# Optimization experiments

Hardware: AMD Instinct MI355X
Metric: run time of the kernel (lower is better)

The kernel has to match this reference:

```python
import jax, jax.numpy as jnp
import numpy as np

# dims
B, T = 64, 512
L = 3                 # number of HMLSTM layers
IN = 512              # per-layer input size (all equal)
D = L * IN            # 1536 total input size
E = 1024              # embedding_size
H1, H2 = 1024, 1024   # linear_sizes
O = 512               # output_size


def setup_inputs() -> dict:
    key = jax.random.key(0)
    ks = jax.random.split(key, 12)
    s = 0.02
    return {
        "x": jax.random.normal(ks[0], (B, T, D), dtype=jnp.float32),
        # gate linears: Linear(sum(input_sizes) -> 1, bias=False), one per layer, stacked [L, D]
        "Wg": jax.random.normal(ks[1], (L, D), dtype=jnp.float32) * s,
        # per-layer embedding linears Linear(IN -> E), stacked [L, E, IN] / [L, E]
        "We": jax.random.normal(ks[2], (L, E, IN), dtype=jnp.float32) * s,
        "be": jax.random.normal(ks[3], (L, E), dtype=jnp.float32) * s,
        # tanh MLP stack
        "W1": jax.random.normal(ks[4], (H1, E), dtype=jnp.float32) * s,
        "b1": jax.random.normal(ks[5], (H1,), dtype=jnp.float32) * s,
        "W2": jax.random.normal(ks[6], (H2, H1), dtype=jnp.float32) * s,
        "b2": jax.random.normal(ks[7], (H2,), dtype=jnp.float32) * s,
        # output head
        "Wo": jax.random.normal(ks[8], (O, H2), dtype=jnp.float32) * s,
        "bo": jax.random.normal(ks[9], (O,), dtype=jnp.float32) * s,
    }


def reference(x, Wg, We, be, W1, b1, W2, b2, Wo, bo):
    b, t, d = x.shape
    h = x.reshape(b * t, d)                       # per-timestep features, fully batched over time
    # gates: sigmoid(Linear(full h -> 1)) per layer -> [N, L]
    g = jax.nn.sigmoid(h @ Wg.T)
    # split full input into per-layer chunks (equal sizes -> reshape) and gate them
    hl = h.reshape(b * t, L, IN) * g[:, :, None]  # [N, L, IN]
    # s = sum_l Linear_l(h_l * g_l); biases sum since each embedding adds its own bias
    s = jnp.einsum("nli,lei->ne", hl, We) + be.sum(axis=0)
    he = jax.nn.relu(s)
    # fnn: tanh-activated linear stack
    o = jnp.tanh(he @ W1.T + b1)
    o = jnp.tanh(o @ W2.T + b2)
    out = o @ Wo.T + bo
    return out.reshape(b, t, O)
```

## Files before the change

### kernel.cpp

```cpp
#include <hip/hip_runtime.h>
#include <math.h>


typedef __attribute__((ext_vector_type(8))) short short8;
typedef __attribute__((ext_vector_type(4))) float float4v;

#define DEV __device__ __forceinline__

DEV unsigned short f2bf(float f){
    union{float f; unsigned int i;} c; c.f = f;
    unsigned int r = c.i + 0x7fffu + ((c.i>>16)&1u);
    return (unsigned short)(r>>16);
}
DEV unsigned int pack2(float a, float b){
    return (unsigned int)f2bf(a) | ((unsigned int)f2bf(b)<<16);
}

DEV void gload_lds16(const unsigned short* g, unsigned short* l){
    __builtin_amdgcn_global_load_lds((const __attribute__((address_space(1))) void*)g,
                                     (__attribute__((address_space(3))) void*)l, 16, 0, 0);
}

__global__ __launch_bounds__(256) void cvt_flat(const float* __restrict__ src,
                                                unsigned short* __restrict__ dst, int n8)
{
    int v = blockIdx.x*256 + threadIdx.x;
    if(v >= n8) return;
    const float4* s = (const float4*)(src) + v*2;
    float4 a = s[0], b = s[1];
    uint4 o;
    o.x = pack2(a.x, a.y); o.y = pack2(a.z, a.w);
    o.z = pack2(b.x, b.y); o.w = pack2(b.z, b.w);
    *((uint4*)dst + v) = o;
}

__global__ __launch_bounds__(256) void cvt_we(const float* __restrict__ We,
                                              unsigned short* __restrict__ Wep)
{
    int v  = blockIdx.x*256 + threadIdx.x;
    int i8 = v & 63;
    int e  = (v>>6) & 1023;
    int l  = v>>16;
    const float4* s = (const float4*)(We + (size_t)l*524288 + (size_t)e*512 + i8*8);
    float4 a = s[0], b = s[1];
    uint4 o;
    o.x = pack2(a.x, a.y); o.y = pack2(a.z, a.w);
    o.z = pack2(b.x, b.y); o.w = pack2(b.z, b.w);
    *(uint4*)(Wep + (size_t)e*1536 + (size_t)l*512 + i8*8) = o;
}

__global__ __launch_bounds__(256) void gate_u(const float* __restrict__ x,
                                              const float* __restrict__ Wg,
                                              unsigned short* __restrict__ u)
{
    int row  = blockIdx.x*4 + (threadIdx.x>>6);
    int lane = threadIdx.x & 63;
    const float4* xr = (const float4*)(x + (size_t)row*1536);
    float4 hv[6];
    #pragma unroll
    for(int j=0;j<6;j++) hv[j] = xr[j*64 + lane];

    float p[3];
    #pragma unroll
    for(int l=0;l<3;l++){
        const float4* wr = (const float4*)(Wg + (size_t)l*1536);
        float s = 0.f;
        #pragma unroll
        for(int j=0;j<6;j++){
            float4 wv = wr[j*64 + lane];
            s += hv[j].x*wv.x + hv[j].y*wv.y + hv[j].z*wv.z + hv[j].w*wv.w;
        }
        p[l] = s;
    }
    #pragma unroll
    for(int off=32; off; off>>=1){
        p[0] += __shfl_xor(p[0], off);
        p[1] += __shfl_xor(p[1], off);
        p[2] += __shfl_xor(p[2], off);
    }
    float g[3];
    #pragma unroll
    for(int l=0;l<3;l++) g[l] = 1.f/(1.f + __expf(-p[l]));

    uint2* ur = (uint2*)(u + (size_t)row*1536);
    #pragma unroll
    for(int j=0;j<6;j++){
        float gj = g[(j*64+lane)>>7];
        uint2 o;
        o.x = pack2(hv[j].x*gj, hv[j].y*gj);
        o.y = pack2(hv[j].z*gj, hv[j].w*gj);
        ur[j*64 + lane] = o;
    }
}

template<int ACT, int BIAS_ROWS, bool F32OUT>
__global__ __launch_bounds__(256) void gemm_bt(
    const unsigned short* __restrict__ A,
    const unsigned short* __restrict__ W,
    const float* __restrict__ bias,
    void* __restrict__ Cv,
    int M, int N, int K)
{
    __shared__ __align__(128) unsigned short As[128*64];
    __shared__ __align__(128) unsigned short Bs[128*64];

    int tid = threadIdx.x;
    int nb  = N >> 7;
    int mt  = M >> 7;
    int xcd = blockIdx.x & 7;
    int j   = blockIdx.x >> 3;
    int bm  = xcd*(mt>>3) + j/nb;
    int bn  = j % nb;
    int m0  = bm << 7, n0 = bn << 7;

    int lane = tid & 63, wv = tid >> 6;
    int wm = wv >> 1, wn = wv & 1;
    int lr = lane & 15, quad = lane >> 4;

    float4v acc[4][4];
    #pragma unroll
    for(int i=0;i<4;i++)
        #pragma unroll
        for(int jj=0;jj<4;jj++) acc[i][jj] = (float4v){0.f,0.f,0.f,0.f};

    int rl  = lane >> 3;
    int cbs = (lane & 7) ^ rl;
    const unsigned short* gA = A + ((size_t)m0 + wv*32 + rl)*K + cbs*8;
    const unsigned short* gB = W + ((size_t)n0 + wv*32 + rl)*K + cbs*8;
    const size_t rstep = (size_t)8*K;

    for(int k0=0; k0<K; k0+=64){
        #pragma unroll
        for(int d=0; d<4; d++){
            gload_lds16(gA + d*rstep, &As[(wv*32 + d*8)*64]);
            gload_lds16(gB + d*rstep, &Bs[(wv*32 + d*8)*64]);
        }
        gA += 64; gB += 64;
        __syncthreads();

        #pragma unroll
        for(int ks=0; ks<2; ks++){
            short8 af[4], bfr[4];
            #pragma unroll
            for(int mi=0;mi<4;mi++){
                int row = wm*64 + mi*16 + lr;
                int cbx = (ks*4 + quad) ^ (lr & 7);
                af[mi] = *(const short8*)(&As[row*64 + cbx*8]);
            }
            #pragma unroll
            for(int ni=0;ni<4;ni++){
                int row = wn*64 + ni*16 + lr;
                int cbx = (ks*4 + quad) ^ (lr & 7);
                bfr[ni] = *(const short8*)(&Bs[row*64 + cbx*8]);
            }
            #pragma unroll
            for(int mi=0;mi<4;mi++)
                #pragma unroll
                for(int ni=0;ni<4;ni++)
                    acc[mi][ni] = __builtin_amdgcn_mfma_f32_16x16x32_bf16(af[mi], bfr[ni], acc[mi][ni], 0, 0, 0);
        }
        __syncthreads();
    }

    #pragma unroll
    for(int ni=0;ni<4;ni++){
        int n = n0 + wn*64 + ni*16 + lr;
        float bsum = 0.f;
        #pragma unroll
        for(int r=0;r<BIAS_ROWS;r++) bsum += bias[(size_t)r*N + n];
        #pragma unroll
        for(int mi=0;mi<4;mi++){
            #pragma unroll
            for(int reg=0;reg<4;reg++){
                int m = m0 + wm*64 + mi*16 + quad*4 + reg;
                float v = acc[mi][ni][reg] + bsum;
                if(ACT==1)      v = fmaxf(v, 0.f);
                else if(ACT==2) v = tanhf(v);
                if constexpr (F32OUT) ((float*)Cv)[(size_t)m*N + n] = v;
                else                  ((unsigned short*)Cv)[(size_t)m*N + n] = f2bf(v);
            }
        }
    }
}

extern "C" void kernel_launch(void* const* d_in, const int* in_sizes, int n_in,
                              void* d_out, int out_size, void* d_ws, size_t ws_size,
                              hipStream_t stream)
{
    const float* x  = (const float*)d_in[0];
    const float* Wg = (const float*)d_in[1];
    const float* We = (const float*)d_in[2];
    const float* be = (const float*)d_in[3];
    const float* W1 = (const float*)d_in[4];
    const float* b1 = (const float*)d_in[5];
    const float* W2 = (const float*)d_in[6];
    const float* b2 = (const float*)d_in[7];
    const float* Wo = (const float*)d_in[8];
    const float* bo = (const float*)d_in[9];
    float* out = (float*)d_out;

    const int M = 32768;

    char* w = (char*)d_ws;
    unsigned short* Wep   = (unsigned short*)w; w += (size_t)1024*1536*2;
    unsigned short* W1b   = (unsigned short*)w; w += (size_t)1024*1024*2;
    unsigned short* W2b   = (unsigned short*)w; w += (size_t)1024*1024*2;
    unsigned short* Wob   = (unsigned short*)w; w += (size_t)512*1024*2;
    unsigned short* slotA = (unsigned short*)w; w += (size_t)M*1536*2;
    unsigned short* slotB = (unsigned short*)w; w += (size_t)M*1024*2;
    unsigned short* u  = slotA;
    unsigned short* o1 = slotA;
    unsigned short* he = slotB;
    unsigned short* o2 = slotB;

    hipLaunchKernelGGL(cvt_flat, dim3(512), dim3(256), 0, stream, W1, W1b, 131072);
    hipLaunchKernelGGL(cvt_flat, dim3(512), dim3(256), 0, stream, W2, W2b, 131072);
    hipLaunchKernelGGL(cvt_flat, dim3(256), dim3(256), 0, stream, Wo, Wob, 65536);
    hipLaunchKernelGGL(cvt_we,   dim3(768), dim3(256), 0, stream, We, Wep);

    hipLaunchKernelGGL(gate_u, dim3(M/4), dim3(256), 0, stream, x, Wg, u);
    hipLaunchKernelGGL((gemm_bt<1,3,false>), dim3((M/128)*(1024/128)), dim3(256), 0, stream,
                       u,  Wep, be, he,  M, 1024, 1536);
    hipLaunchKernelGGL((gemm_bt<2,1,false>), dim3((M/128)*(1024/128)), dim3(256), 0, stream,
                       he, W1b, b1, o1,  M, 1024, 1024);
    hipLaunchKernelGGL((gemm_bt<2,1,false>), dim3((M/128)*(1024/128)), dim3(256), 0, stream,
                       o1, W2b, b2, o2,  M, 1024, 1024);
    hipLaunchKernelGGL((gemm_bt<0,1,true>),  dim3((M/128)*(512/128)),  dim3(256), 0, stream,
                       o2, Wob, bo, out, M, 512, 1024);
}
```

Measured before the change: 729.0 us.

## Replace GEMM with 256x256 tiled, double-buffered, 8-wave pipelined kernel

Replaces the 128x128 single-buffered GEMM with a 256x256 tile kernel using 512 threads and two LDS stages. Global-to-LDS loads for the next one or two K steps are issued in chunks between MFMA groups, with fine-grained barriers, vmcnt waits and setprio. The aim is to hide memory latency behind MFMA work and raise data reuse per tile. The cost is more LDS per block (128 KB) and more register pressure, which may lower occupancy. The manual barrier and waitcnt ordering also needs care to stay correct.

```diff
diff --git a/kernel.cpp b/kernel.cpp
--- a/kernel.cpp
+++ b/kernel.cpp
@@ -94,86 +94,111 @@
 }
 
 template<int ACT, int BIAS_ROWS, bool F32OUT>
-__global__ __launch_bounds__(256) void gemm_bt(
+__global__ __launch_bounds__(512, 2) void gemm256(
     const unsigned short* __restrict__ A,
     const unsigned short* __restrict__ W,
     const float* __restrict__ bias,
     void* __restrict__ Cv,
     int M, int N, int K)
 {
-    __shared__ __align__(128) unsigned short As[128*64];
-    __shared__ __align__(128) unsigned short Bs[128*64];
-
-    int tid = threadIdx.x;
-    int nb  = N >> 7;
-    int mt  = M >> 7;
-    int xcd = blockIdx.x & 7;
-    int j   = blockIdx.x >> 3;
-    int bm  = xcd*(mt>>3) + j/nb;
-    int bn  = j % nb;
-    int m0  = bm << 7, n0 = bn << 7;
-
-    int lane = tid & 63, wv = tid >> 6;
-    int wm = wv >> 1, wn = wv & 1;
-    int lr = lane & 15, quad = lane >> 4;
-
-    float4v acc[4][4];
-    #pragma unroll
-    for(int i=0;i<4;i++)
+    __shared__ __align__(128) unsigned short As[2*2*128*64];
+    __shared__ __align__(128) unsigned short Bs[2*2*128*64];
+
+    const int tid = threadIdx.x;
+    const int nb  = N >> 8;
+    const int mt  = M >> 8;
+    const int xcd = blockIdx.x & 7;
+    const int j   = blockIdx.x >> 3;
+    const int bm  = xcd*(mt>>3) + j/nb;
+    const int bn  = j % nb;
+    const int m0  = bm << 8, n0 = bn << 8;
+
+    const int lane = tid & 63, wid = tid >> 6;
+    const int wm = wid >> 2, wn = wid & 3;
+    const int lr = lane & 15, quad = lane >> 4, sx = lr & 7;
+    const int srow = lane >> 3;
+    const int scb  = (lane & 7) ^ srow;
+    const size_t aoff = (size_t)srow*K + scb*8;
+    const int nt = K >> 6;
+
+    float4v acc[8][4];
+    #pragma unroll
+    for(int i=0;i<8;i++)
         #pragma unroll
         for(int jj=0;jj<4;jj++) acc[i][jj] = (float4v){0.f,0.f,0.f,0.f};
 
-    int rl  = lane >> 3;
-    int cbs = (lane & 7) ^ rl;
-    const unsigned short* gA = A + ((size_t)m0 + wv*32 + rl)*K + cbs*8;
-    const unsigned short* gB = W + ((size_t)n0 + wv*32 + rl)*K + cbs*8;
-    const size_t rstep = (size_t)8*K;
-
-    for(int k0=0; k0<K; k0+=64){
-        #pragma unroll
-        for(int d=0; d<4; d++){
-            gload_lds16(gA + d*rstep, &As[(wv*32 + d*8)*64]);
-            gload_lds16(gB + d*rstep, &Bs[(wv*32 + d*8)*64]);
+#define STAGE_A(h,l,s) gload_lds16(A + ((size_t)(m0 + (h)*128 + (l)*64 + wid*8))*K + (s)*64 + aoff, \
+                                   &As[(((s)&1)*2+(h))*8192 + ((l)*64 + wid*8)*64])
+#define STAGE_B(h,l,s) gload_lds16(W + ((size_t)(n0 + (h)*128 + (l)*64 + wid*8))*K + (s)*64 + aoff, \
+                                   &Bs[(((s)&1)*2+(h))*8192 + ((l)*64 + wid*8)*64])
+
+    STAGE_A(0,0,0); STAGE_A(0,1,0); STAGE_A(1,0,0); STAGE_A(1,1,0);
+    STAGE_B(0,0,0); STAGE_B(0,1,0); STAGE_B(1,0,0); STAGE_B(1,1,0);
+    if(nt > 1){
+        STAGE_B(0,0,1); STAGE_B(0,1,1); STAGE_B(1,0,1); STAGE_B(1,1,1);
+        STAGE_A(0,0,1); STAGE_A(1,0,1);
+        asm volatile("s_waitcnt vmcnt(6)" ::: "memory");
+    } else {
+        asm volatile("s_waitcnt vmcnt(0)" ::: "memory");
+    }
+    __builtin_amdgcn_s_barrier();
+
+    for(int t=0; t<nt; ++t){
+        const int cur = t & 1;
+        const unsigned short* Ab = &As[(cur*2 + wm)*8192];
+        const unsigned short* Bb = &Bs[(cur*2 + (wn>>1))*8192 + (wn&1)*4096];
+        short8 bfr[4][2];
+        #pragma unroll
+        for(int q=0; q<4; ++q){
+            short8 af[2][2];
+            #pragma unroll
+            for(int mi=0; mi<2; ++mi)
+                #pragma unroll
+                for(int ks=0; ks<2; ++ks)
+                    af[mi][ks] = *(const short8*)&Ab[(q*32 + mi*16 + lr)*64 + (((ks*4+quad)^sx)*8)];
+            if(q==0){
+                #pragma unroll
+                for(int ni=0; ni<4; ++ni)
+                    #pragma unroll
+                    for(int ks=0; ks<2; ++ks)
+                        bfr[ni][ks] = *(const short8*)&Bb[(ni*16 + lr)*64 + (((ks*4+quad)^sx)*8)];
+            }
+            if(q==0)      { if(t+1 < nt){ STAGE_A(0,1,t+1); STAGE_A(1,1,t+1); } }
+            else if(q==1) { if(t+2 < nt){ STAGE_B(0,0,t+2); STAGE_B(0,1,t+2); } }
+            else if(q==2) { if(t+2 < nt){ STAGE_B(1,0,t+2); STAGE_B(1,1,t+2); } }
+            else          { if(t+2 < nt){ STAGE_A(0,0,t+2); STAGE_A(1,0,t+2); } }
+            __builtin_amdgcn_s_barrier();
+            __builtin_amdgcn_s_setprio(1);
+            #pragma unroll
+            for(int ks=0; ks<2; ++ks)
+                #pragma unroll
+                for(int mi=0; mi<2; ++mi)
+                    #pragma unroll
+                    for(int ni=0; ni<4; ++ni)
+                        acc[q*2+mi][ni] = __builtin_amdgcn_mfma_f32_16x16x32_bf16(
+                            af[mi][ks], bfr[ni][ks], acc[q*2+mi][ni], 0, 0, 0);
+            __builtin_amdgcn_s_setprio(0);
+            if(q < 3) __builtin_amdgcn_s_barrier();
         }
-        gA += 64; gB += 64;
-        __syncthreads();
-
-        #pragma unroll
-        for(int ks=0; ks<2; ks++){
-            short8 af[4], bfr[4];
+        if(t+2 < nt) asm volatile("s_waitcnt vmcnt(6)" ::: "memory");
+        else         asm volatile("s_waitcnt vmcnt(0)" ::: "memory");
+        __builtin_amdgcn_s_barrier();
+    }
+#undef STAGE_A
+#undef STAGE_B
+
+    #pragma unroll
+    for(int ni=0; ni<4; ++ni){
+        const int n = n0 + wn*64 + ni*16 + lr;
+        float bsum = 0.f;
+        #pragma unroll
+        for(int r=0; r<BIAS_ROWS; ++r) bsum += bias[(size_t)r*N + n];
+        #pragma unroll
+        for(int Q=0; Q<8; ++Q){
             #pragma unroll
-            for(int mi=0;mi<4;mi++){
-                int row = wm*64 + mi*16 + lr;
-                int cbx = (ks*4 + quad) ^ (lr & 7);
-                af[mi] = *(const short8*)(&As[row*64 + cbx*8]);
-            }
-            #pragma unroll
-            for(int ni=0;ni<4;ni++){
-                int row = wn*64 + ni*16 + lr;
-                int cbx = (ks*4 + quad) ^ (lr & 7);
-                bfr[ni] = *(const short8*)(&Bs[row*64 + cbx*8]);
-            }
-            #pragma unroll
-            for(int mi=0;mi<4;mi++)
-                #pragma unroll
-                for(int ni=0;ni<4;ni++)
-                    acc[mi][ni] = __builtin_amdgcn_mfma_f32_16x16x32_bf16(af[mi], bfr[ni], acc[mi][ni], 0, 0, 0);
-        }
-        __syncthreads();
-    }
-
-    #pragma unroll
-    for(int ni=0;ni<4;ni++){
-        int n = n0 + wn*64 + ni*16 + lr;
-        float bsum = 0.f;
-        #pragma unroll
-        for(int r=0;r<BIAS_ROWS;r++) bsum += bias[(size_t)r*N + n];
-        #pragma unroll
-        for(int mi=0;mi<4;mi++){
-            #pragma unroll
-            for(int reg=0;reg<4;reg++){
-                int m = m0 + wm*64 + mi*16 + quad*4 + reg;
-                float v = acc[mi][ni][reg] + bsum;
+            for(int reg=0; reg<4; ++reg){
+                const int m = m0 + wm*128 + Q*16 + quad*4 + reg;
+                float v = acc[Q][ni][reg] + bsum;
                 if(ACT==1)      v = fmaxf(v, 0.f);
                 else if(ACT==2) v = tanhf(v);
                 if constexpr (F32OUT) ((float*)Cv)[(size_t)m*N + n] = v;
@@ -219,12 +244,12 @@
     hipLaunchKernelGGL(cvt_we,   dim3(768), dim3(256), 0, stream, We, Wep);
 
     hipLaunchKernelGGL(gate_u, dim3(M/4), dim3(256), 0, stream, x, Wg, u);
-    hipLaunchKernelGGL((gemm_bt<1,3,false>), dim3((M/128)*(1024/128)), dim3(256), 0, stream,
+    hipLaunchKernelGGL((gemm256<1,3,false>), dim3((M/256)*(1024/256)), dim3(512), 0, stream,
                        u,  Wep, be, he,  M, 1024, 1536);
-    hipLaunchKernelGGL((gemm_bt<2,1,false>), dim3((M/128)*(1024/128)), dim3(256), 0, stream,
+    hipLaunchKernelGGL((gemm256<2,1,false>), dim3((M/256)*(1024/256)), dim3(512), 0, stream,
                        he, W1b, b1, o1,  M, 1024, 1024);
-    hipLaunchKernelGGL((gemm_bt<2,1,false>), dim3((M/128)*(1024/128)), dim3(256), 0, stream,
+    hipLaunchKernelGGL((gemm256<2,1,false>), dim3((M/256)*(1024/256)), dim3(512), 0, stream,
                        o1, W2b, b2, o2,  M, 1024, 1024);
-    hipLaunchKernelGGL((gemm_bt<0,1,true>),  dim3((M/128)*(512/128)),  dim3(256), 0, stream,
+    hipLaunchKernelGGL((gemm256<0,1,true>),  dim3((M/256)*(512/256)),  dim3(512), 0, stream,
                        o2, Wob, bo, out, M, 512, 1024);
 }
```

Result: faster. 684.3 us (-6.1%).
